# Optimization experiments

Hardware: AMD Instinct MI355X
Metric: run time of the kernel (lower is better)

Reference implementation:

```python
import jax, jax.numpy as jnp
import numpy as np

# dims
T, B, N, H = 16, 8, 8, 128            # time, batch, num_schemas, schema_dim
C, IH, IW = 32, 16, 16                # conv_dims
TASK, ACT, REW = 128, 16, 1
HEADS = 7
TAR = TASK + ACT + REW                # 145
CTX = H + TAR                         # 273 context_dim
CONV_FLAT = C * IH * IW               # 8192
MEM_IN = CONV_FLAT + H + CTX          # 8593


def setup_inputs() -> dict:
    key = jax.random.key(0)
    ks = jax.random.split(key, 20)
    def n(k, shape, s=0.02):
        return jax.random.normal(k, shape, dtype=jnp.float32) * s
    D = HEADS * H
    return {
        "image": jax.random.normal(ks[0], (T, B, C, IH, IW), dtype=jnp.float32),
        "task_action_reward": jax.random.normal(ks[1], (T, B, TAR), dtype=jnp.float32),
        # MultiHeadedAttention params
        "Wq_w": n(ks[2], (D, CTX)), "Wq_b": jnp.zeros((D,), jnp.float32),
        "Wk_w": n(ks[3], (D, H)),   "Wk_b": jnp.zeros((D,), jnp.float32),
        "Wv_w": n(ks[4], (D, H)),   "Wv_b": jnp.zeros((D,), jnp.float32),
        "Wo_w": n(ks[5], (H, D)),   "Wo_b": jnp.zeros((H,), jnp.float32),
        # TopdownFeatureAttention: N per-query linears (stacked) + 1x1 conv
        "td_w": n(ks[6], (N, C, CTX)), "td_b": jnp.zeros((N, C), jnp.float32),
        "conv_w": n(ks[7], (C, C)), "conv_b": jnp.zeros((C,), jnp.float32),
        # ListStructuredRnn: N per-schema LSTM cells (PyTorch gate order i,f,g,o)
        "Wih": n(ks[8], (N, 4 * H, MEM_IN)), "Whh": n(ks[9], (N, 4 * H, H)),
        "bih": jnp.zeros((N, 4 * H), jnp.float32), "bhh": jnp.zeros((N, 4 * H), jnp.float32),
    }


def reference(image, task_action_reward, Wq_w, Wq_b, Wk_w, Wk_b, Wv_w, Wv_b,
              Wo_w, Wo_b, td_w, td_b, conv_w, conv_b, Wih, Whh, bih, bhh):
    f32 = image.dtype
    # prev_state=None path: prev_h is zeros for all timesteps
    prev_h = jnp.zeros((T, B, N, H), f32)
    # schema_context = duplicate task_action_reward over schemas, cat prev_h -> (T,B,N,CTX)
    ctx = jnp.concatenate(
        [jnp.broadcast_to(task_action_reward[:, :, None, :], (T, B, N, TAR)), prev_h], axis=-1)
    # keys = cat(prev_h, zeros) along schema axis -> (T,B,N+1,H)
    keys = jnp.concatenate([prev_h, jnp.zeros((T, B, 1, H), f32)], axis=2)

    # --- MultiHeadedAttention (no mask; dropout unused in forward) ---
    q = (ctx @ Wq_w.T + Wq_b).reshape(T, B, N, HEADS, H)
    k = (keys @ Wk_w.T + Wk_b).reshape(T, B, N + 1, HEADS, H)
    v = (keys @ Wv_w.T + Wv_b).reshape(T, B, N + 1, HEADS, H)
    scores = jnp.einsum('tbqhd,tbkhd->tbhqk', q, k) / jnp.sqrt(jnp.asarray(H, f32))
    attn = jax.nn.softmax(scores, axis=-1)
    xatt = jnp.einsum('tbhqk,tbkhd->tbqhd', attn, v).reshape(T, B, N, HEADS * H)
    shared = xatt @ Wo_w.T + Wo_b                      # (T,B,N,H)

    # --- TopdownFeatureAttention: per-query linear -> sigmoid channel gate -> 1x1 conv ---
    gate = jax.nn.sigmoid(jnp.einsum('tbnx,ncx->tbnc', ctx, td_w) + td_b)   # (T,B,N,C)
    modulated = image[:, :, None] * gate[..., None, None]                    # (T,B,N,C,IH,IW)
    conv = jnp.einsum('tbnchw,dc->tbndhw', modulated, conv_w) + conv_b[:, None, None]
    schema_updates = conv.reshape(T, B, N, CONV_FLAT)

    # --- per-schema LSTMs over time (zero initial state) ---
    mem = jnp.concatenate([schema_updates, shared, ctx], axis=-1)            # (T,B,N,MEM_IN)
    xg = jnp.einsum('tbni,ngi->tbng', mem, Wih) + bih + bhh                  # (T,B,N,4H)

    def step(carry, g_t):
        h, c = carry
        g = g_t + jnp.einsum('bnh,ngh->bng', h, Whh)
        i, f, gg, o = jnp.split(g, 4, axis=-1)
        c = jax.nn.sigmoid(f) * c + jax.nn.sigmoid(i) * jnp.tanh(gg)
        h = jax.nn.sigmoid(o) * jnp.tanh(c)
        return (h, c), h

    z = jnp.zeros((B, N, H), f32)
    (hT, cT), hs = jax.lax.scan(step, (z, z), xg)
    outs = hs.reshape(T, B, N * H)
    return outs, hT, cT
```

## Files before the change

### kernel.cpp

```cpp
#include <hip/hip_runtime.h>

#define T_   16
#define B_   8
#define N_   8
#define H_   128
#define C_   32
#define HW_  256
#define TAR_ 145
#define G4H  512
#define MEMIN 8593
#define AK   8512
#define XGN  524288
#define KSTEP 64

typedef __attribute__((ext_vector_type(8))) short short8v;
typedef __attribute__((ext_vector_type(4))) float f32x4;
typedef __attribute__((ext_vector_type(4), aligned(4))) float f32x4u;

__device__ __forceinline__ float bf2f(unsigned short u){
  return __uint_as_float(((unsigned int)u) << 16);
}
__device__ __forceinline__ unsigned short f2bf(float x){
  unsigned int b = __float_as_uint(x);
  return (unsigned short)((b + 0x7fffu + ((b >> 16) & 1u)) >> 16);
}
__device__ __forceinline__ unsigned pkbf(float lo, float hi){
  return __builtin_amdgcn_perm(__float_as_uint(hi) + 0x8000u,
                               __float_as_uint(lo) + 0x8000u, 0x07060302u);
}
__device__ __forceinline__ float bflo(unsigned w){ return __uint_as_float(w << 16); }
__device__ __forceinline__ float bfhi(unsigned w){ return __uint_as_float(w & 0xffff0000u); }
__device__ __forceinline__ float sigf(float x){ return 1.f/(1.f + expf(-x)); }

__device__ __forceinline__ void gl_lds16(const void* g, void* l){
  __builtin_amdgcn_global_load_lds(
      (const __attribute__((address_space(1))) unsigned int*)g,
      (__attribute__((address_space(3))) unsigned int*)l, 16, 0, 0);
}
__device__ __forceinline__ void gl_lds4(const void* g, void* l){
  __builtin_amdgcn_global_load_lds(
      (const __attribute__((address_space(1))) unsigned int*)g,
      (__attribute__((address_space(3))) unsigned int*)l, 4, 0, 0);
}

__global__ void k_shared(const float* __restrict__ WvB, const float* __restrict__ WoW,
                         const float* __restrict__ WoB, float* __restrict__ sh){
  const int h = blockIdx.x, lane = threadIdx.x;
  float acc = 0.f;
  for(int d = lane; d < 896; d += 64) acc += WvB[d] * WoW[h*896 + d];
  for(int s = 32; s; s >>= 1) acc += __shfl_down(acc, s);
  if(lane == 0) sh[h] = acc + WoB[h];
}

__global__ __launch_bounds__(256) void k_conv3(
    const float* __restrict__ img, const float* __restrict__ tar,
    const float* __restrict__ tdw, const float* __restrict__ tdb,
    const float* __restrict__ cw, const float* __restrict__ cb,
    const float* __restrict__ sh, unsigned short* __restrict__ mem)
{
  __shared__ float imgS[8192];
  __shared__ float cwgT[1024];
  __shared__ float tarS[160];
  __shared__ float gateS[32];
  const int bid = blockIdx.x;
  const int n = bid & 7, tb = bid >> 3;
  const int hw = threadIdx.x;

  if(hw < 145) tarS[hw] = tar[tb*TAR_ + hw];
  for(int i = hw; i < 8192; i += 256)
    imgS[i] = img[(size_t)tb*8192 + i];
  __syncthreads();
  if(hw < 32){
    float a = tdb[n*32 + hw];
    const float* tw = tdw + (size_t)(n*32 + hw)*273;
    #pragma unroll 5
    for(int x = 0; x < 145; ++x) a += tarS[x]*tw[x];
    gateS[hw] = sigf(a);
  }
  __syncthreads();
  for(int i = hw; i < 1024; i += 256){
    const int c = i >> 5, d = i & 31;
    cwgT[i] = cw[d*32 + c] * gateS[c];
  }
  __syncthreads();

  f32x4 acc[8];
  #pragma unroll
  for(int dq = 0; dq < 8; ++dq){
    const f32x4u cv = *(const f32x4u*)&cb[dq*4];
    acc[dq].x = cv.x; acc[dq].y = cv.y; acc[dq].z = cv.z; acc[dq].w = cv.w;
  }
  #pragma unroll 4
  for(int c = 0; c < 32; ++c){
    const float iv = imgS[c*256 + hw];
    #pragma unroll
    for(int dq = 0; dq < 8; ++dq){
      const f32x4 w = *(const f32x4*)&cwgT[c*32 + dq*4];
      acc[dq].x += iv*w.x; acc[dq].y += iv*w.y;
      acc[dq].z += iv*w.z; acc[dq].w += iv*w.w;
    }
  }
  unsigned short* mrow = mem + (size_t)(n*128 + tb)*AK;
  #pragma unroll
  for(int dq = 0; dq < 8; ++dq){
    mrow[(dq*4 + 0)*256 + hw] = f2bf(acc[dq].x);
    mrow[(dq*4 + 1)*256 + hw] = f2bf(acc[dq].y);
    mrow[(dq*4 + 2)*256 + hw] = f2bf(acc[dq].z);
    mrow[(dq*4 + 3)*256 + hw] = f2bf(acc[dq].w);
  }
  for(int i = hw; i < 320; i += 256){
    if(i < 128)      mrow[8192 + i]       = f2bf(sh[i]);
    else if(i < 273) mrow[8320 + i - 128] = f2bf(tarS[i - 128]);
    else             mrow[8465 + i - 273] = 0;
  }
}

__global__ __launch_bounds__(256) void k_gemm5x(
    const unsigned short* __restrict__ mem, const float* __restrict__ Wih,
    float* __restrict__ xg4)
{
  __shared__ unsigned short Abuf[2][128*64];
  __shared__ float          Bbuf[2][16*64];
  const int bid = blockIdx.x;
  const int n = bid & 7;
  const int r2 = bid >> 3;
  const int gt = r2 & 31, ks = r2 >> 5;
  const int tid = threadIdx.x;
  const int wv = tid >> 6, ln = tid & 63;
  const int lr = ln & 15, lg = ln >> 4;
  const int g0 = gt*16;
  const int kbeg = (ks == 0) ? 0 : 2176 + (ks - 1)*2112;
  const int nsteps = (ks == 0) ? 34 : 33;
  const unsigned short* An = mem + (size_t)n*128*AK;
  const float* Bn = Wih + (size_t)(n*G4H + g0)*MEMIN;

#define STAGE5(bb, kk) do{                                                     \
    _Pragma("unroll")                                                          \
    for(int i_ = 0; i_ < 4; ++i_){                                             \
      const int ci_ = i_*256 + tid;                                            \
      const int row_ = ci_ >> 3;                                               \
      const unsigned short* src_ = An + (size_t)row_*AK + (kk)                 \
                                   + (((ci_ & 7) ^ (row_ & 7)) << 3);          \
      gl_lds16(src_, &Abuf[bb][(i_*256 + wv*64)*8]);                           \
    }                                                                          \
    _Pragma("unroll")                                                          \
    for(int q_ = 0; q_ < 4; ++q_){                                             \
      const int idx_ = q_*256 + tid;                                           \
      const int g_ = idx_ >> 6;                                                \
      const int kd_ = idx_ & 63;                                               \
      const float* srcB_ = Bn + (size_t)g_*MEMIN + (kk)                        \
                           + ((((kd_ >> 3) ^ (g_ & 7)) << 3) + (kd_ & 7));     \
      gl_lds4(srcB_, &Bbuf[bb][q_*256 + wv*64]);                               \
    }                                                                          \
  }while(0)

  f32x4 acc0 = {0.f,0.f,0.f,0.f};
  f32x4 acc1 = {0.f,0.f,0.f,0.f};

  STAGE5(0, kbeg);
  if(nsteps > 1) STAGE5(1, kbeg + KSTEP);

  int b = 0;
  for(int t = 0; t < nsteps; ++t){
    if(t < nsteps - 1){
      asm volatile("s_waitcnt vmcnt(8)" ::: "memory");
    } else {
      asm volatile("s_waitcnt vmcnt(0)" ::: "memory");
    }
    __builtin_amdgcn_s_barrier();
    #pragma unroll
    for(int s = 0; s < 2; ++s){
      const int jb = (s*4 + lg) ^ (lr & 7);
      const float* bp = &Bbuf[b][lr*64 + jb*8];
      const f32x4 blo = *(const f32x4*)bp;
      const f32x4 bhi = *(const f32x4*)(bp + 4);
      short8v bf;
      unsigned* u = (unsigned*)&bf;
      u[0] = pkbf(blo.x, blo.y); u[1] = pkbf(blo.z, blo.w);
      u[2] = pkbf(bhi.x, bhi.y); u[3] = pkbf(bhi.z, bhi.w);
      const short8v a0 = *(const short8v*)&Abuf[b][(wv*32 + lr)*64 + jb*8];
      const short8v a1 = *(const short8v*)&Abuf[b][(wv*32 + 16 + lr)*64 + jb*8];
      acc0 = __builtin_amdgcn_mfma_f32_16x16x32_bf16(a0, bf, acc0, 0, 0, 0);
      acc1 = __builtin_amdgcn_mfma_f32_16x16x32_bf16(a1, bf, acc1, 0, 0, 0);
    }
    __builtin_amdgcn_s_barrier();
    if(t + 2 < nsteps) STAGE5(b, kbeg + (t+2)*KSTEP);
    b ^= 1;
  }
#undef STAGE5

  float* dst = xg4 + (size_t)ks*XGN;
  const int c0 = g0 + lr;
  const int r0 = wv*32 + lg*4, r1 = r0 + 16;
  #pragma unroll
  for(int j = 0; j < 4; ++j){
    dst[(size_t)((r0 + j)*8 + n)*G4H + c0] = acc0[j];
    dst[(size_t)((r1 + j)*8 + n)*G4H + c0] = acc1[j];
  }
}

__global__ __launch_bounds__(512) void k_lstm2(
    const float* __restrict__ xg4, int nsum, const float* __restrict__ Whh,
    const float* __restrict__ bih, const float* __restrict__ bhh,
    float* __restrict__ out)
{
  __shared__ float hS[128];
  __shared__ float preS[512];
  const int bn = blockIdx.x;
  const int n = bn & 7, b = bn >> 3;
  const int g = threadIdx.x;

  unsigned wr[64];
  const float* wrow = Whh + (size_t)(n*G4H + g)*H_;
  #pragma unroll
  for(int i = 0; i < 32; ++i){
    const f32x4 w = *(const f32x4*)(wrow + i*4);
    wr[2*i]   = pkbf(w.x, w.y);
    wr[2*i+1] = pkbf(w.z, w.w);
  }
  const float bias = bih[n*G4H + g] + bhh[n*G4H + g];
  if(g < 128) hS[g] = 0.f;
  float cc = 0.f;
  __syncthreads();

  for(int t = 0; t < 16; ++t){
    const size_t xb = (size_t)((t*8 + b)*8 + n)*G4H + g;
    float acc = bias;
    for(int u = 0; u < nsum; ++u) acc += xg4[xb + (size_t)u*XGN];
    #pragma unroll
    for(int q = 0; q < 32; ++q){
      const f32x4 hv = *(const f32x4*)&hS[q*4];
      const unsigned w0 = wr[2*q], w1 = wr[2*q+1];
      acc += hv.x*bflo(w0) + hv.y*bfhi(w0) + hv.z*bflo(w1) + hv.w*bfhi(w1);
    }
    preS[g] = acc;
    __syncthreads();
    if(g < 128){
      const float iv = sigf(preS[g]);
      const float fv = sigf(preS[128 + g]);
      const float gv = tanhf(preS[256 + g]);
      const float ov = sigf(preS[384 + g]);
      cc = fv*cc + iv*gv;
      const float hn = ov*tanhf(cc);
      hS[g] = hn;
      out[(t*8 + b)*1024 + n*128 + g] = hn;
      if(t == 15){
        out[131072 + (b*8 + n)*128 + g] = hn;
        out[139264 + (b*8 + n)*128 + g] = cc;
      }
    }
    __syncthreads();
  }
}

extern "C" void kernel_launch(void* const* d_in, const int* in_sizes, int n_in,
                              void* d_out, int out_size, void* d_ws, size_t ws_size,
                              hipStream_t stream)
{
  (void)in_sizes; (void)n_in; (void)out_size; (void)ws_size;
  const float* img  = (const float*)d_in[0];
  const float* tar  = (const float*)d_in[1];
  const float* WvB  = (const float*)d_in[7];
  const float* WoW  = (const float*)d_in[8];
  const float* WoB  = (const float*)d_in[9];
  const float* tdw  = (const float*)d_in[10];
  const float* tdb  = (const float*)d_in[11];
  const float* cw   = (const float*)d_in[12];
  const float* cb   = (const float*)d_in[13];
  const float* Wih  = (const float*)d_in[14];
  const float* Whh  = (const float*)d_in[15];
  const float* bih  = (const float*)d_in[16];
  const float* bhh  = (const float*)d_in[17];

  float* wsf = (float*)d_ws;
  float* shw = wsf + 32768;
  float* xgw = wsf + 32896;
  unsigned short* memA = (unsigned short*)((char*)d_ws + 8520192);

  k_shared<<<128, 64, 0, stream>>>(WvB, WoW, WoB, shw);
  k_conv3<<<1024, 256, 0, stream>>>(img, tar, tdw, tdb, cw, cb, shw, memA);
  k_gemm5x<<<1024, 256, 0, stream>>>(memA, Wih, xgw);
  k_lstm2<<<64, 512, 0, stream>>>(xgw, 4, Whh, bih, bhh, (float*)d_out);
}
```

Measured before the change: 117.8 us.

## Add wider-tile split-K input-projection GEMM with eight K-splits

Adds a new GEMM kernel for the LSTM input projection. Each block computes 64 gate columns instead of 16, so every staged activation tile in LDS is reused across four waves, and K is split eight ways instead of four. It uses 72 KB of dynamic shared memory, double-buffered, with swizzled A loads and padded B rows. The LSTM kernel then sums 8 partial results, and the old path stays as a fallback when the workspace is too small. The trade-offs are fewer blocks (512), higher LDS use per block that limits occupancy, and more partial-sum traffic.

```diff
diff --git a/kernel.cpp b/kernel.cpp
--- a/kernel.cpp
+++ b/kernel.cpp
@@ -112,6 +112,94 @@
     if(i < 128)      mrow[8192 + i]       = f2bf(sh[i]);
     else if(i < 273) mrow[8320 + i - 128] = f2bf(tarS[i - 128]);
     else             mrow[8465 + i - 273] = 0;
+  }
+}
+
+__global__ __launch_bounds__(256) void k_gemm10(
+    const unsigned short* __restrict__ mem, const float* __restrict__ Wih,
+    float* __restrict__ xg8)
+{
+  extern __shared__ char sm10[];
+  unsigned short (*Abuf)[8192] = (unsigned short(*)[8192])sm10;
+  float (*Bbuf)[5120] = (float(*)[5120])(sm10 + 2*16384);
+  const int n = blockIdx.x, gt = blockIdx.y, ks = blockIdx.z;
+  const int tid = threadIdx.x;
+  const int wv = tid >> 6, ln = tid & 63;
+  const int lr = ln & 15, lg = ln >> 4;
+  const int g0 = gt*64;
+  const int nsteps = (ks < 5) ? 17 : 16;
+  const int kbeg = 64 * ((ks < 5) ? 17*ks : 85 + 16*(ks - 5));
+  const unsigned short* An = mem + (size_t)n*128*AK;
+  const int rbase = n*512 + g0 + wv*16;
+
+#define STAGE10(bb, kk) do{                                                    \
+    _Pragma("unroll")                                                          \
+    for(int i_ = 0; i_ < 4; ++i_){                                             \
+      const int ci_ = i_*256 + tid;                                            \
+      const int row_ = ci_ >> 3;                                               \
+      gl_lds16(An + (size_t)row_*AK + (kk) + (((ci_ & 7) ^ (row_ & 7)) << 3),  \
+               (char*)&Abuf[bb][0] + (i_*256 + wv*64)*16);                     \
+    }                                                                          \
+    _Pragma("unroll")                                                          \
+    for(int o_ = 0; o_ < 5; ++o_){                                             \
+      const int p_ = o_*64 + ln;                                               \
+      int gl_ = p_ / 18;                                                       \
+      const int c_ = p_ - gl_*18;                                              \
+      if(gl_ > 15) gl_ = 15;                                                   \
+      const size_t ridx_ = (size_t)(rbase + gl_);                              \
+      const char* src_ = (const char*)Wih + ridx_*((size_t)MEMIN*4)            \
+                         + (size_t)(kk)*4 - ((ridx_ & 3)*4) + c_*16;           \
+      gl_lds16(src_, (char*)&Bbuf[bb][0] + wv*5120 + o_*1024);                 \
+    }                                                                          \
+  }while(0)
+
+  f32x4 acc[8];
+  #pragma unroll
+  for(int rt = 0; rt < 8; ++rt){ acc[rt].x=0.f; acc[rt].y=0.f; acc[rt].z=0.f; acc[rt].w=0.f; }
+
+  STAGE10(0, kbeg);
+  if(nsteps > 1) STAGE10(1, kbeg + KSTEP);
+
+  int b = 0;
+  for(int t = 0; t < nsteps; ++t){
+    if(t < nsteps - 1){
+      asm volatile("s_waitcnt vmcnt(9)" ::: "memory");
+    } else {
+      asm volatile("s_waitcnt vmcnt(0)" ::: "memory");
+    }
+    __builtin_amdgcn_s_barrier();
+    const char* Ab = (const char*)&Abuf[b][0];
+    #pragma unroll
+    for(int s = 0; s < 2; ++s){
+      const int u = s*4 + lg;
+      const int fb = wv*1280 + lr*72 + (lr & 3) + u*8;
+      const f32x4u blo = *(const f32x4u*)&Bbuf[b][fb];
+      const f32x4u bhi = *(const f32x4u*)&Bbuf[b][fb + 4];
+      short8v bf;
+      unsigned* up = (unsigned*)&bf;
+      up[0] = pkbf(blo.x, blo.y); up[1] = pkbf(blo.z, blo.w);
+      up[2] = pkbf(bhi.x, bhi.y); up[3] = pkbf(bhi.z, bhi.w);
+      const int jbx = u ^ (lr & 7);
+      #pragma unroll
+      for(int rt = 0; rt < 8; ++rt){
+        const short8v a = *(const short8v*)(Ab + (((rt*16 + lr)*8 + jbx) << 4));
+        acc[rt] = __builtin_amdgcn_mfma_f32_16x16x32_bf16(a, bf, acc[rt], 0, 0, 0);
+      }
+    }
+    __builtin_amdgcn_s_barrier();
+    if(t + 2 < nsteps) STAGE10(b, kbeg + (t + 2)*KSTEP);
+    b ^= 1;
+  }
+#undef STAGE10
+
+  float* dst = xg8 + (size_t)ks*XGN;
+  const int col = g0 + wv*16 + lr;
+  #pragma unroll
+  for(int rt = 0; rt < 8; ++rt){
+    #pragma unroll
+    for(int j = 0; j < 4; ++j){
+      dst[(size_t)((rt*16 + lg*4 + j)*8 + n)*G4H + col] = acc[rt][j];
+    }
   }
 }
 
@@ -257,7 +345,7 @@
                               void* d_out, int out_size, void* d_ws, size_t ws_size,
                               hipStream_t stream)
 {
-  (void)in_sizes; (void)n_in; (void)out_size; (void)ws_size;
+  (void)in_sizes; (void)n_in; (void)out_size;
   const float* img  = (const float*)d_in[0];
   const float* tar  = (const float*)d_in[1];
   const float* WvB  = (const float*)d_in[7];
@@ -275,10 +363,23 @@
   float* wsf = (float*)d_ws;
   float* shw = wsf + 32768;
   float* xgw = wsf + 32896;
-  unsigned short* memA = (unsigned short*)((char*)d_ws + 8520192);
+
+  unsigned short* memA8 = (unsigned short*)((char*)d_ws + 16908800);
+  const size_t WS_A8 = 16908800 + (size_t)8*128*AK*2;
+
+  unsigned short* memB4 = (unsigned short*)((char*)d_ws + 8520192);
 
   k_shared<<<128, 64, 0, stream>>>(WvB, WoW, WoB, shw);
-  k_conv3<<<1024, 256, 0, stream>>>(img, tar, tdw, tdb, cw, cb, shw, memA);
-  k_gemm5x<<<1024, 256, 0, stream>>>(memA, Wih, xgw);
-  k_lstm2<<<64, 512, 0, stream>>>(xgw, 4, Whh, bih, bhh, (float*)d_out);
-}
+
+  if(ws_size >= WS_A8){
+    k_conv3<<<1024, 256, 0, stream>>>(img, tar, tdw, tdb, cw, cb, shw, memA8);
+    (void)hipFuncSetAttribute((const void*)k_gemm10,
+                              hipFuncAttributeMaxDynamicSharedMemorySize, 73728);
+    k_gemm10<<<dim3(8, 8, 8), 256, 73728, stream>>>(memA8, Wih, xgw);
+    k_lstm2<<<64, 512, 0, stream>>>(xgw, 8, Whh, bih, bhh, (float*)d_out);
+  } else {
+    k_conv3<<<1024, 256, 0, stream>>>(img, tar, tdw, tdb, cw, cb, shw, memB4);
+    k_gemm5x<<<1024, 256, 0, stream>>>(memB4, Wih, xgw);
+    k_lstm2<<<64, 512, 0, stream>>>(xgw, 4, Whh, bih, bhh, (float*)d_out);
+  }
+}
```

Result: slower. 123.9 us (+5.2%).

## Add register-staged double-buffered A loads in xg GEMM kernel

Applied to the files above, without the earlier changes.

Adds a new GEMM kernel that prefetches the bf16 activation tile two K-steps ahead into registers, writes it into the alternate LDS buffer, and streams the fp32 weight tile into LDS by direct global-to-LDS loads. This is meant to hide global-load latency behind the MFMA work on the current buffer. The new kernel is chosen when the workspace is large enough, and the old kernel remains as a fallback. The gain costs extra registers for the staged A data plus two barriers per step.

```diff
diff --git a/kernel.cpp b/kernel.cpp
--- a/kernel.cpp
+++ b/kernel.cpp
@@ -112,6 +112,118 @@
     if(i < 128)      mrow[8192 + i]       = f2bf(sh[i]);
     else if(i < 273) mrow[8320 + i - 128] = f2bf(tarS[i - 128]);
     else             mrow[8465 + i - 273] = 0;
+  }
+}
+
+__global__ __launch_bounds__(256) void k_gemm11(
+    const unsigned short* __restrict__ mem, const float* __restrict__ Wih,
+    float* __restrict__ xg4)
+{
+  __shared__ unsigned short Abuf[2][128*64];
+  __shared__ float          Bbuf[2][16*64];
+  const int bid = blockIdx.x;
+  const int n = bid & 7;
+  const int r2 = bid >> 3;
+  const int gt = r2 & 31, ks = r2 >> 5;
+  const int tid = threadIdx.x;
+  const int wv = tid >> 6, ln = tid & 63;
+  const int lr = ln & 15, lg = ln >> 4;
+  const int g0 = gt*16;
+  const int kbeg = (ks == 0) ? 0 : 2176 + (ks - 1)*2112;
+  const int nsteps = (ks == 0) ? 34 : 33;
+  const unsigned short* An = mem + (size_t)n*128*AK;
+  const float* Bn = Wih + (size_t)(n*G4H + g0)*MEMIN;
+
+  uint4 rP[4], rQ[4];
+
+#define LOADA(dst, kk) do{                                                     \
+    _Pragma("unroll")                                                          \
+    for(int i_ = 0; i_ < 4; ++i_){                                             \
+      const int ci_ = i_*256 + tid;                                            \
+      const int row_ = ci_ >> 3;                                               \
+      dst[i_] = *(const uint4*)(An + (size_t)row_*AK + (kk)                    \
+                                + (((ci_ & 7) ^ (row_ & 7)) << 3));            \
+    }                                                                          \
+  }while(0)
+
+#define WRITEA(bb, src) do{                                                    \
+    _Pragma("unroll")                                                          \
+    for(int i_ = 0; i_ < 4; ++i_){                                             \
+      *(uint4*)&Abuf[bb][(i_*256 + tid)*8] = src[i_];                          \
+    }                                                                          \
+  }while(0)
+
+#define BDMA(bb, kk) do{                                                       \
+    _Pragma("unroll")                                                          \
+    for(int q_ = 0; q_ < 4; ++q_){                                             \
+      const int idx_ = q_*256 + tid;                                           \
+      const int g_ = idx_ >> 6;                                                \
+      const int kd_ = idx_ & 63;                                               \
+      const float* srcB_ = Bn + (size_t)g_*MEMIN + (kk)                        \
+                           + ((((kd_ >> 3) ^ (g_ & 7)) << 3) + (kd_ & 7));     \
+      gl_lds4(srcB_, &Bbuf[bb][q_*256 + wv*64]);                               \
+    }                                                                          \
+  }while(0)
+
+  f32x4 acc0 = {0.f,0.f,0.f,0.f};
+  f32x4 acc1 = {0.f,0.f,0.f,0.f};
+
+  LOADA(rQ, kbeg);
+  BDMA(0, kbeg);
+  if(nsteps > 1){
+    LOADA(rP, kbeg + KSTEP);
+    BDMA(1, kbeg + KSTEP);
+    asm volatile("s_waitcnt vmcnt(8)" ::: "memory");
+  } else {
+    asm volatile("s_waitcnt vmcnt(0)" ::: "memory");
+  }
+  WRITEA(0, rQ);
+  asm volatile("s_waitcnt lgkmcnt(0)" ::: "memory");
+  __builtin_amdgcn_s_barrier();
+
+  int b = 0;
+  for(int t = 0; t < nsteps; ++t){
+    #pragma unroll
+    for(int s = 0; s < 2; ++s){
+      const int jb = (s*4 + lg) ^ (lr & 7);
+      const float* bp = &Bbuf[b][lr*64 + jb*8];
+      const f32x4 blo = *(const f32x4*)bp;
+      const f32x4 bhi = *(const f32x4*)(bp + 4);
+      short8v bf;
+      unsigned* u = (unsigned*)&bf;
+      u[0] = pkbf(blo.x, blo.y); u[1] = pkbf(blo.z, blo.w);
+      u[2] = pkbf(bhi.x, bhi.y); u[3] = pkbf(bhi.z, bhi.w);
+      const short8v a0 = *(const short8v*)&Abuf[b][(wv*32 + lr)*64 + jb*8];
+      const short8v a1 = *(const short8v*)&Abuf[b][(wv*32 + 16 + lr)*64 + jb*8];
+      acc0 = __builtin_amdgcn_mfma_f32_16x16x32_bf16(a0, bf, acc0, 0, 0, 0);
+      acc1 = __builtin_amdgcn_mfma_f32_16x16x32_bf16(a1, bf, acc1, 0, 0, 0);
+    }
+    const bool more2 = (t + 2 < nsteps);
+    if(more2) LOADA(rQ, kbeg + (t + 2)*KSTEP);
+    __builtin_amdgcn_s_barrier();
+    if(t + 1 < nsteps){
+      if(more2) BDMA(b, kbeg + (t + 2)*KSTEP);
+      if(more2){ asm volatile("s_waitcnt vmcnt(8)" ::: "memory"); }
+      else     { asm volatile("s_waitcnt vmcnt(0)" ::: "memory"); }
+      WRITEA(b^1, rP);
+      #pragma unroll
+      for(int i = 0; i < 4; ++i){ uint4 tmp = rP[i]; rP[i] = rQ[i]; rQ[i] = tmp; }
+      asm volatile("s_waitcnt lgkmcnt(0)" ::: "memory");
+    }
+    __builtin_amdgcn_s_barrier();
+    b ^= 1;
+  }
+#undef LOADA
+#undef WRITEA
+#undef BDMA
+
+  float* dst = xg4 + (size_t)ks*XGN;
+  const int c0 = g0 + lr;
+  const int r0 = wv*32 + lg*4, r1 = r0 + 16;
+  #pragma unroll
+  for(int j = 0; j < 4; ++j){
+    dst[(size_t)((r0 + j)*8 + n)*G4H + c0] = acc0[j];
+    dst[(size_t)((r1 + j)*8 + n)*G4H + c0] = acc1[j];
   }
 }
 
@@ -257,7 +369,7 @@
                               void* d_out, int out_size, void* d_ws, size_t ws_size,
                               hipStream_t stream)
 {
-  (void)in_sizes; (void)n_in; (void)out_size; (void)ws_size;
+  (void)in_sizes; (void)n_in; (void)out_size;
   const float* img  = (const float*)d_in[0];
   const float* tar  = (const float*)d_in[1];
   const float* WvB  = (const float*)d_in[7];
@@ -276,9 +388,14 @@
   float* shw = wsf + 32768;
   float* xgw = wsf + 32896;
   unsigned short* memA = (unsigned short*)((char*)d_ws + 8520192);
+  const size_t WS_A = 8520192 + (size_t)8*128*AK*2;
 
   k_shared<<<128, 64, 0, stream>>>(WvB, WoW, WoB, shw);
   k_conv3<<<1024, 256, 0, stream>>>(img, tar, tdw, tdb, cw, cb, shw, memA);
-  k_gemm5x<<<1024, 256, 0, stream>>>(memA, Wih, xgw);
+  if(ws_size >= WS_A){
+    k_gemm11<<<1024, 256, 0, stream>>>(memA, Wih, xgw);
+  } else {
+    k_gemm5x<<<1024, 256, 0, stream>>>(memA, Wih, xgw);
+  }
   k_lstm2<<<64, 512, 0, stream>>>(xgw, 4, Whh, bih, bhh, (float*)d_out);
 }
```

New measurement: 121.5 us. +3.1%, slower.
